# Kernel optimization log

Measured on AMD Instinct MI355X. Metric: run time of the kernel, lower is better.

## Reference

```python
import jax, jax.numpy as jnp
import numpy as np

DIM = 384
HEADS = 12
WIN = (7, 7)
N = WIN[0] * WIN[1]
B = 4096
NW = 64  # number of windows sharing one mask


def _relative_position_index(win):
    wh, ww = win
    coords = np.stack(np.meshgrid(np.arange(wh), np.arange(ww), indexing='ij'))  # (2,wh,ww)
    flat = coords.reshape(2, -1)                                                 # (2, N)
    rel = flat[:, :, None] - flat[:, None, :]                                    # (2, N, N)
    rel = rel.transpose(1, 2, 0).astype(np.int64)
    rel[:, :, 0] += wh - 1
    rel[:, :, 1] += ww - 1
    rel[:, :, 0] *= 2 * ww - 1
    return jnp.asarray(rel.sum(-1), dtype=jnp.int32)                             # (N, N)


def setup_inputs() -> dict:
    key = jax.random.key(0)
    ks = jax.random.split(key, 7)
    std = 0.02
    return {
        'x': jax.random.normal(ks[0], (B, N, DIM), jnp.float32),
        'mask': jax.random.normal(ks[1], (NW, N, N), jnp.float32),
        'qkv_w': jax.random.normal(ks[2], (3 * DIM, DIM), jnp.float32) * std,
        'qkv_b': jnp.zeros((3 * DIM,), jnp.float32),
        'bias_table': jax.random.normal(ks[3], ((2 * WIN[0] - 1) * (2 * WIN[1] - 1), HEADS), jnp.float32) * std,
        'proj_w': jax.random.normal(ks[4], (DIM, DIM), jnp.float32) * std,
        'proj_b': jnp.zeros((DIM,), jnp.float32),
        'rel_idx': _relative_position_index(WIN),
    }


def reference(x, mask, qkv_w, qkv_b, bias_table, proj_w, proj_b, rel_idx):
    B_, n, c = x.shape
    h = HEADS
    d = c // h
    scale = d ** -0.5

    qkv = x @ qkv_w.T + qkv_b                                  # (B_, N, 3C)
    qkv = qkv.reshape(B_, n, 3, h, d).transpose(2, 0, 3, 1, 4)  # (3, B_, H, N, D)
    q, k, v = qkv[0], qkv[1], qkv[2]

    attn = jnp.einsum('bhnd,bhmd->bhnm', q, k) * scale          # (B_, H, N, N)

    bias = bias_table[rel_idx]                                  # (N, N, H)
    attn = attn + bias.transpose(2, 0, 1)[None]                 # add (1, H, N, N)

    nW = mask.shape[0]
    attn = attn.reshape(B_ // nW, nW, h, n, n) + mask[None, :, None]
    attn = attn.reshape(B_, h, n, n)

    attn = jax.nn.softmax(attn, axis=-1)
    out = jnp.einsum('bhnm,bhmd->bhnd', attn, v)                # (B_, H, N, D)
    out = out.transpose(0, 2, 1, 3).reshape(B_, n, c)
    return out @ proj_w.T + proj_b
```

## Files before the change

kernel.cpp:

```cpp
#include <hip/hip_runtime.h>

typedef __bf16 bf16;
typedef __bf16 bf16x4 __attribute__((ext_vector_type(4)));
typedef __bf16 bf16x8 __attribute__((ext_vector_type(8)));
typedef float f32x4 __attribute__((ext_vector_type(4)));
typedef float f32x16 __attribute__((ext_vector_type(16)));
typedef int i32x2 __attribute__((ext_vector_type(2)));
typedef unsigned int u32;

#define DIMC 384
#define NHEADS 12
#define NTOK 49
#define NWINB 4096
#define MROWS (NWINB*NTOK)

#define MFMA32(A,B,C) __builtin_amdgcn_mfma_f32_32x32x16_bf16(A,B,C,0,0,0)

#define GLOAD16(gsrc, lbase) \
  __builtin_amdgcn_global_load_lds( \
      (const __attribute__((address_space(1))) u32*)(gsrc), \
      (__attribute__((address_space(3))) u32*)(lbase), 16, 0, 0)

__global__ __launch_bounds__(256) void k_convert(const float4* __restrict__ in,
                                                 bf16x4* __restrict__ out, int n4) {
  int stride = gridDim.x * blockDim.x;
  for (int i = blockIdx.x * blockDim.x + threadIdx.x; i < n4; i += stride) {
    float4 v = in[i];
    bf16x4 o;
    o[0] = (bf16)v.x; o[1] = (bf16)v.y; o[2] = (bf16)v.z; o[3] = (bf16)v.w;
    out[i] = o;
  }
}

__global__ __launch_bounds__(256) void k_zero(float4* __restrict__ p, int n4) {
  int stride = gridDim.x * blockDim.x;
  float4 z = {0.f, 0.f, 0.f, 0.f};
  for (int i = blockIdx.x * blockDim.x + threadIdx.x; i < n4; i += stride) p[i] = z;
}

__global__ __launch_bounds__(256) void k_bm(const float* __restrict__ table,
                                            const int* __restrict__ rel,
                                            const float* __restrict__ mask,
                                            float* __restrict__ outp) {
  int i = blockIdx.x * 256 + threadIdx.x;
  if (i < NHEADS * 64 * NTOK * NTOK) {
    int hw = i / 2401, r2 = i - hw * 2401;
    int h = hw >> 6, w = hw & 63;
    int key = r2 / NTOK, q = r2 - key * NTOK;
    outp[i] = table[rel[q * NTOK + key] * NHEADS + h] + mask[(w * NTOK + q) * NTOK + key];
  }
}

template <int MODE>
__global__ __launch_bounds__(256) void k_gemm(const bf16* __restrict__ A,
                                              const bf16* __restrict__ Bw,
                                              const float* __restrict__ bias,
                                              bf16* __restrict__ oQ, bf16* __restrict__ oK,
                                              bf16* __restrict__ oV, float* __restrict__ oP) {
  __shared__ __align__(16) bf16 lA[2][64 * 64];
  __shared__ __align__(16) bf16 lB[2][128 * 64];
  const int t = threadIdx.x;
  const int l = t & 63;
  const int wv = t >> 6;
  const int wr = wv >> 1, wc = wv & 1;

  const u32 NXB = MODE == 0 ? 9 : 3;
  const u32 nwg = NXB * (MROWS / 64);
  u32 lin = blockIdx.y * gridDim.x + blockIdx.x;
  u32 logical = (lin & 7) * (nwg >> 3) + (lin >> 3);
  const int n0 = (int)(logical % NXB) * 128;
  const int m0 = (int)(logical / NXB) * 64;

  const int lr = l & 15, lg = l >> 4;

  const int srowA = wv * 16 + (l >> 3);
  const int srowB = wv * 32 + (l >> 3);
  const int scolb = (l & 7) * 16;

  f32x4 acc[2][4] = {};

#define STAGE(BUF, K0)                                                            \
  {                                                                               \
    _Pragma("unroll") for (int i = 0; i < 2; ++i) {                               \
      int row = srowA + i * 8;                                                    \
      int sc = (scolb ^ ((row & 7) << 4)) >> 1;                                   \
      GLOAD16(&A[(size_t)(m0 + row) * DIMC + (K0) + sc],                          \
              &lA[BUF][wv * 1024 + i * 512]);                                     \
    }                                                                             \
    _Pragma("unroll") for (int i = 0; i < 4; ++i) {                               \
      int row = srowB + i * 8;                                                    \
      int sc = (scolb ^ ((row & 7) << 4)) >> 1;                                   \
      GLOAD16(&Bw[(size_t)(n0 + row) * DIMC + (K0) + sc],                         \
              &lB[BUF][wv * 2048 + i * 512]);                                     \
    }                                                                             \
  }

  STAGE(0, 0);

#pragma unroll
  for (int tt = 0; tt < 6; ++tt) {
    const int cur = tt & 1;
    if (tt > 0) __builtin_amdgcn_s_barrier();
    if (tt < 5) {
      STAGE(cur ^ 1, (tt + 1) * 64);
      asm volatile("s_waitcnt vmcnt(6)" ::: "memory");
    } else {
      asm volatile("s_waitcnt vmcnt(0)" ::: "memory");
    }
    __builtin_amdgcn_s_barrier();

#pragma unroll
    for (int kk = 0; kk < 64; kk += 32) {
      bf16x8 af[2], bfv[4];
#pragma unroll
      for (int f = 0; f < 2; ++f) {
        int row = wr * 32 + f * 16 + lr;
        int cb = (kk + lg * 8) * 2;
        af[f] = *reinterpret_cast<const bf16x8*>(
            &lA[cur][row * 64 + ((cb ^ ((row & 7) << 4)) >> 1)]);
      }
#pragma unroll
      for (int f = 0; f < 4; ++f) {
        int row = wc * 64 + f * 16 + lr;
        int cb = (kk + lg * 8) * 2;
        bfv[f] = *reinterpret_cast<const bf16x8*>(
            &lB[cur][row * 64 + ((cb ^ ((row & 7) << 4)) >> 1)]);
      }
#pragma unroll
      for (int fm = 0; fm < 2; ++fm)
#pragma unroll
        for (int fn = 0; fn < 4; ++fn)
          acc[fm][fn] = __builtin_amdgcn_mfma_f32_16x16x32_bf16(af[fm], bfv[fn], acc[fm][fn], 0, 0, 0);
    }
  }
#undef STAGE

  const int cbase = n0 + wc * 64;
  if (MODE == 0) {
    const int which = cbase / 384;
    const int colh = cbase - which * 384;
#pragma unroll
    for (int fn = 0; fn < 4; ++fn) {
      const int cc = colh + fn * 16 + lr;
      const int h = cc >> 5, d = cc & 31;
      const float bc = bias[cbase + fn * 16 + lr];
#pragma unroll
      for (int fm = 0; fm < 2; ++fm) {
#pragma unroll
        for (int r = 0; r < 4; ++r) {
          const int m = m0 + wr * 32 + fm * 16 + lg * 4 + r;
          const int bi = m / 49, n = m - bi * 49;
          const size_t p = (size_t)bi * 12 + h;
          const float v = acc[fm][fn][r] + bc;
          if (which < 2) {
            bf16* dst = which == 0 ? oQ : oK;
            dst[(p * 49 + n) * 32 + d] = (bf16)v;
          } else {
            oV[p * 2048 + d * 64 + n] = (bf16)v;
          }
        }
      }
    }
  } else {
#pragma unroll
    for (int fn = 0; fn < 4; ++fn) {
      const int c = cbase + fn * 16 + lr;
      const float bc = bias[c];
#pragma unroll
      for (int fm = 0; fm < 2; ++fm) {
#pragma unroll
        for (int r = 0; r < 4; ++r) {
          const int m = m0 + wr * 32 + fm * 16 + lg * 4 + r;
          oP[(size_t)m * 384 + c] = acc[fm][fn][r] + bc;
        }
      }
    }
  }
}

__global__ __launch_bounds__(256, 4) void k_attn(const bf16* __restrict__ Q,
                                                 const bf16* __restrict__ K,
                                                 const bf16* __restrict__ VT,
                                                 const float* __restrict__ bmT,
                                                 bf16* __restrict__ H) {
  const int t = threadIdx.x, l = t & 63, wv = t >> 6;
  const int p = blockIdx.x * 4 + wv;
  const int b = p / 12, h = p - b * 12;
  const int w = b & 63;
  const size_t base = (size_t)p * (49 * 32);
  const int c = l & 31, b5 = l >> 5;

  bf16x8 vf[4];
#pragma unroll
  for (int kk = 0; kk < 4; ++kk)
    vf[kk] = *reinterpret_cast<const bf16x8*>(&VT[(size_t)p * 2048 + c * 64 + kk * 16 + b5 * 8]);

  bf16x8 kf[2][2], qf[2][2];
#pragma unroll
  for (int f = 0; f < 2; ++f) {
    int row = f * 32 + c; if (row > 48) row = 48;
#pragma unroll
    for (int kd = 0; kd < 2; ++kd) {
      kf[f][kd] = *reinterpret_cast<const bf16x8*>(&K[base + row * 32 + kd * 16 + b5 * 8]);
      qf[f][kd] = *reinterpret_cast<const bf16x8*>(&Q[base + row * 32 + kd * 16 + b5 * 8]);
    }
  }

  const float scale = 0.17677669529663689f;
  const float* bm = bmT + ((size_t)h * 64 + w) * 2401;

#pragma unroll
  for (int fn = 0; fn < 2; ++fn) {
    f32x16 s0 = {}, s1 = {};
    s0 = MFMA32(kf[0][0], qf[fn][0], s0);
    s0 = MFMA32(kf[0][1], qf[fn][1], s0);
    s1 = MFMA32(kf[1][0], qf[fn][0], s1);
    s1 = MFMA32(kf[1][1], qf[fn][1], s1);

    int q = fn * 32 + c;
    int qc = q > 48 ? 48 : q;

    float vals[32];
    float vmax = -1e30f;
#pragma unroll
    for (int fm = 0; fm < 2; ++fm) {
#pragma unroll
      for (int r = 0; r < 16; ++r) {
        int key = fm * 32 + (r & 3) + 8 * (r >> 2) + 4 * b5;
        float sv = fm ? s1[r] : s0[r];
        float v;
        if (key < 49) {
          v = fmaf(sv, scale, bm[key * 49 + qc]);
        } else {
          v = -1e30f;
        }
        vals[fm * 16 + r] = v;
        vmax = fmaxf(vmax, v);
      }
    }
    vmax = fmaxf(vmax, __shfl_xor(vmax, 32));
    float sum = 0.f;
#pragma unroll
    for (int i = 0; i < 32; ++i) {
      float e = __expf(vals[i] - vmax);
      vals[i] = e;
      sum += e;
    }
    sum += __shfl_xor(sum, 32);
    float inv = 1.f / sum;

    f32x16 o = {};
#pragma unroll
    for (int kk = 0; kk < 4; ++kk) {
      int ib = (kk >> 1) * 16 + 8 * (kk & 1);
      union { bf16 hh[2]; u32 u; } cv;
      u32 A0, A1, B0, B1;
      cv.hh[0] = (bf16)(vals[ib + 0] * inv); cv.hh[1] = (bf16)(vals[ib + 1] * inv); A0 = cv.u;
      cv.hh[0] = (bf16)(vals[ib + 2] * inv); cv.hh[1] = (bf16)(vals[ib + 3] * inv); A1 = cv.u;
      cv.hh[0] = (bf16)(vals[ib + 4] * inv); cv.hh[1] = (bf16)(vals[ib + 5] * inv); B0 = cv.u;
      cv.hh[0] = (bf16)(vals[ib + 6] * inv); cv.hh[1] = (bf16)(vals[ib + 7] * inv); B1 = cv.u;
      i32x2 sw0 = __builtin_amdgcn_permlane32_swap((int)A0, (int)B0, false, false);
      i32x2 sw1 = __builtin_amdgcn_permlane32_swap((int)A1, (int)B1, false, false);
      union { u32 d[4]; bf16x8 v8; } pa;
      pa.d[0] = (u32)sw0[0]; pa.d[1] = (u32)sw1[0];
      pa.d[2] = (u32)sw0[1]; pa.d[3] = (u32)sw1[1];
      o = MFMA32(pa.v8, vf[kk], o);
    }

#pragma unroll
    for (int r = 0; r < 16; ++r) {
      int qrow = fn * 32 + (r & 3) + 8 * (r >> 2) + 4 * b5;
      if (qrow < 49)
        H[((size_t)b * 49 + qrow) * 384 + h * 32 + c] = (bf16)o[r];
    }
  }
}

extern "C" void kernel_launch(void* const* d_in, const int* in_sizes, int n_in,
                              void* d_out, int out_size, void* d_ws, size_t ws_size,
                              hipStream_t stream) {
  const float* x     = (const float*)d_in[0];
  const float* mask  = (const float*)d_in[1];
  const float* qkvw  = (const float*)d_in[2];
  const float* qkvb  = (const float*)d_in[3];
  const float* btab  = (const float*)d_in[4];
  const float* projw = (const float*)d_in[5];
  const float* projb = (const float*)d_in[6];
  const int*   rel   = (const int*)d_in[7];
  float* out = (float*)d_out;

  const size_t NB  = 154140672;
  const size_t VTB = 201326592;
  const size_t BMB = 7375872;
  char* ws = (char*)d_ws;
  bf16*  xb    = (bf16*)ws;
  bf16*  vT    = (bf16*)(ws + NB);
  float* bmT   = (float*)(ws + NB + VTB);
  bf16*  wqkv  = (bf16*)(ws + NB + VTB + BMB);
  bf16*  wproj = (bf16*)(ws + NB + VTB + BMB + 884736);
  bf16* qb = (bf16*)d_out;
  bf16* kb = qb + NB / 2;

  k_convert<<<2048, 256, 0, stream>>>((const float4*)x, (bf16x4*)xb, (int)(NB / 8));
  k_convert<<<432, 256, 0, stream>>>((const float4*)qkvw, (bf16x4*)wqkv, 3 * DIMC * DIMC / 4);
  k_convert<<<144, 256, 0, stream>>>((const float4*)projw, (bf16x4*)wproj, DIMC * DIMC / 4);
  k_bm<<<(NHEADS * 64 * NTOK * NTOK + 255) / 256, 256, 0, stream>>>(btab, rel, mask, bmT);
  k_zero<<<2048, 256, 0, stream>>>((float4*)vT, (int)(VTB / 16));

  k_gemm<0><<<dim3(9, MROWS / 64), 256, 0, stream>>>(xb, wqkv, qkvb, qb, kb, vT, nullptr);
  k_attn<<<(NWINB * NHEADS) / 4, 256, 0, stream>>>(qb, kb, vT, bmT, xb);
  k_gemm<1><<<dim3(3, MROWS / 64), 256, 0, stream>>>(xb, wproj, projb, nullptr, nullptr, nullptr, out);
}
```

Measured before the change: 947.2 us.

## Transpose V epilogue through LDS and zero only padding columns of vT

```diff
diff --git a/kernel.cpp b/kernel.cpp
--- a/kernel.cpp
+++ b/kernel.cpp
@@ -32,10 +32,11 @@
   }
 }
 
-__global__ __launch_bounds__(256) void k_zero(float4* __restrict__ p, int n4) {
-  int stride = gridDim.x * blockDim.x;
+__global__ __launch_bounds__(256) void k_padzero(bf16* __restrict__ vT) {
+  int i = blockIdx.x * 256 + threadIdx.x;
   float4 z = {0.f, 0.f, 0.f, 0.f};
-  for (int i = blockIdx.x * blockDim.x + threadIdx.x; i < n4; i += stride) p[i] = z;
+  float4* p = reinterpret_cast<float4*>(vT + (size_t)i * 64 + 48);
+  p[0] = z; p[1] = z;
 }
 
 __global__ __launch_bounds__(256) void k_bm(const float* __restrict__ table,
@@ -136,27 +137,50 @@
 #undef STAGE
 
   const int cbase = n0 + wc * 64;
-  if (MODE == 0) {
-    const int which = cbase / 384;
-    const int colh = cbase - which * 384;
-#pragma unroll
-    for (int fn = 0; fn < 4; ++fn) {
-      const int cc = colh + fn * 16 + lr;
-      const int h = cc >> 5, d = cc & 31;
-      const float bc = bias[cbase + fn * 16 + lr];
-#pragma unroll
-      for (int fm = 0; fm < 2; ++fm) {
-#pragma unroll
-        for (int r = 0; r < 4; ++r) {
-          const int m = m0 + wr * 32 + fm * 16 + lg * 4 + r;
-          const int bi = m / 49, n = m - bi * 49;
-          const size_t p = (size_t)bi * 12 + h;
-          const float v = acc[fm][fn][r] + bc;
-          if (which < 2) {
-            bf16* dst = which == 0 ? oQ : oK;
-            dst[(p * 49 + n) * 32 + d] = (bf16)v;
-          } else {
-            oV[p * 2048 + d * 64 + n] = (bf16)v;
+  if constexpr (MODE == 0) {
+    if (n0 >= 768) {
+      __shared__ __align__(4) bf16 et[64 * 130];
+#pragma unroll
+      for (int fn = 0; fn < 4; ++fn) {
+        const float bc = bias[cbase + fn * 16 + lr];
+        const int col = wc * 64 + fn * 16 + lr;
+#pragma unroll
+        for (int fm = 0; fm < 2; ++fm) {
+#pragma unroll
+          for (int r = 0; r < 4; ++r) {
+            const int row = wr * 32 + fm * 16 + lg * 4 + r;
+            et[row * 130 + col] = (bf16)(acc[fm][fn][r] + bc);
+          }
+        }
+      }
+      __syncthreads();
+      const int vbase = n0 - 768;
+      const int m = m0 + l;
+      const int bi = m / 49, n = m - bi * 49;
+#pragma unroll
+      for (int cc = 0; cc < 32; ++cc) {
+        const int col = wv * 32 + cc;
+        const bf16 val = et[l * 130 + col];
+        const int vcol = vbase + col;
+        const int h = vcol >> 5, d = vcol & 31;
+        oV[((size_t)bi * 12 + h) * 2048 + d * 64 + n] = val;
+      }
+    } else {
+      const int which = cbase / 384;
+      const int colh = cbase - which * 384;
+      bf16* dst = which == 0 ? oQ : oK;
+#pragma unroll
+      for (int fn = 0; fn < 4; ++fn) {
+        const int cc = colh + fn * 16 + lr;
+        const int h = cc >> 5, d = cc & 31;
+        const float bc = bias[cbase + fn * 16 + lr];
+#pragma unroll
+        for (int fm = 0; fm < 2; ++fm) {
+#pragma unroll
+          for (int r = 0; r < 4; ++r) {
+            const int m = m0 + wr * 32 + fm * 16 + lg * 4 + r;
+            const int bi = m / 49, n = m - bi * 49;
+            dst[(((size_t)bi * 12 + h) * 49 + n) * 32 + d] = (bf16)(acc[fm][fn][r] + bc);
           }
         }
       }
@@ -305,7 +329,7 @@
   k_convert<<<432, 256, 0, stream>>>((const float4*)qkvw, (bf16x4*)wqkv, 3 * DIMC * DIMC / 4);
   k_convert<<<144, 256, 0, stream>>>((const float4*)projw, (bf16x4*)wproj, DIMC * DIMC / 4);
   k_bm<<<(NHEADS * 64 * NTOK * NTOK + 255) / 256, 256, 0, stream>>>(btab, rel, mask, bmT);
-  k_zero<<<2048, 256, 0, stream>>>((float4*)vT, (int)(VTB / 16));
+  k_padzero<<<6144, 256, 0, stream>>>(vT);
 
   k_gemm<0><<<dim3(9, MROWS / 64), 256, 0, stream>>>(xb, wqkv, qkvb, qb, kb, vT, nullptr);
   k_attn<<<(NWINB * NHEADS) / 4, 256, 0, stream>>>(qb, kb, vT, bmT, xb);
```

New measurement: 965.7 us. Within noise of the previous version (+2.0%).
